# Kernel tuning notes

Hardware: AMD Instinct MI355X
Metric: run time of the kernel (lower is better)

Reference implementation:

```python
import jax, jax.numpy as jnp
import numpy as np

EPS_CLAMP = 1e-6
TAU2 = 1.0


def _l2norm_rows(x):
    # F.normalize(x, p=2, dim=1) with eps=1e-12
    n = jnp.sqrt(jnp.sum(x * x, axis=1, keepdims=True))
    return x / jnp.maximum(n, 1e-12)


def _ws_v22(x_mean, x_std):
    m = _l2norm_rows(x_mean)                      # [N, F]
    c = _l2norm_rows(jnp.exp(x_std))              # [N, F]
    sq = jnp.sum(m * m, axis=1)                   # [N]
    # squared euclidean pairwise distance (cdist(...)**2)
    d2 = jnp.maximum(sq[:, None] + sq[None, :] - 2.0 * (m @ m.T), 0.0)
    csum = jnp.sum(c, axis=1)                     # [N]
    cs = jnp.sqrt(c)
    res = d2 + csum[:, None] + csum[None, :] - 2.0 * (cs @ cs.T)
    return jnp.exp(-res)                          # [N, N]


def _gcn_conv_dense(A, x, W, b):
    # PyG GCNConv with dense weighted adjacency A (A[i,j] = weight of edge i->j),
    # add_remaining_self_loops(fill=1), deg over target (column sums),
    # norm_ij = d_i^-1/2 * A_ij * d_j^-1/2, aggregate at target: out = A_norm^T @ (xW) + b
    diag = jnp.diagonal(A)
    A = A + jnp.diag(jnp.where(diag > 0, 0.0, 1.0))  # add self-loop weight 1 only where missing
    deg = jnp.sum(A, axis=0)                         # column sums (target degree)
    dis = jnp.where(deg > 0, deg ** -0.5, 0.0)
    An = dis[:, None] * A * dis[None, :]
    return An.T @ (x @ W) + b


def _encoder(A, x, W0, b0, W1, b1):
    h = jax.nn.relu(_gcn_conv_dense(A, x, W0, b0))
    return jax.nn.relu(_gcn_conv_dense(A, h, W1, b1))


def setup_inputs() -> dict:
    key = jax.random.key(0)
    ks = jax.random.split(key, 16)
    N, F, H = 4096, 512, 256
    s_in = 1.0 / np.sqrt(F)
    s_h = 1.0 / np.sqrt(2 * H)
    inp = {
        "x": jax.random.normal(ks[0], (N, F), dtype=jnp.float32),
        "new_edge": jax.random.uniform(ks[1], (N, N), dtype=jnp.float32),
        "beta": jax.random.uniform(ks[2], (1,), dtype=jnp.float32),
        "delta": jax.random.uniform(ks[3], (1,), dtype=jnp.float32),
        "eps": jax.random.uniform(ks[4], (N, N), dtype=jnp.float32),
        "Wm": jax.random.uniform(ks[5], (F, F), jnp.float32, -s_in, s_in),
        "bm": jax.random.uniform(ks[6], (F,), jnp.float32, -s_in, s_in),
        "Ws": jax.random.uniform(ks[7], (F, F), jnp.float32, -s_in, s_in),
        "bs": jax.random.uniform(ks[8], (F,), jnp.float32, -s_in, s_in),
        "mW0": jax.random.uniform(ks[9], (F, 2 * H), jnp.float32, -s_in, s_in) ,
        "mb0": jnp.zeros((2 * H,), jnp.float32),
        "mW1": jax.random.uniform(ks[10], (2 * H, H), jnp.float32, -s_h, s_h),
        "mb1": jnp.zeros((H,), jnp.float32),
        "sW0": jax.random.uniform(ks[11], (F, 2 * H), jnp.float32, -s_in, s_in),
        "sb0": jnp.zeros((2 * H,), jnp.float32),
        "sW1": jax.random.uniform(ks[12], (2 * H, H), jnp.float32, -s_h, s_h),
        "sb1": jnp.zeros((H,), jnp.float32),
    }
    return inp


def reference(x, new_edge, beta, delta, eps, Wm, bm, Ws, bs,
              mW0, mb0, mW1, mb1, sW0, sb0, sW1, sb1):
    b = beta[0]
    d = delta[0]
    x_mean = x @ Wm + bm
    x_std = x @ Ws + bs
    ws = _l2norm_rows(_ws_v22(x_mean, x_std))       # F.normalize(WS_v22(...)) row-wise
    term = (1.0 - b) * ws + b * new_edge
    term = jnp.clip(term, EPS_CLAMP, 1.0 - EPS_CLAMP)
    term = jnp.log(term / (1.0 - term))
    e = jnp.clip(eps, EPS_CLAMP, 1.0 - EPS_CLAMP)
    term = term + jnp.log(e / (1.0 - e))
    term = jax.nn.sigmoid(term / TAU2)
    term = jnp.where(term > d, term, 0.0)           # dense sparsified adjacency
    z_mean = _encoder(term, x_mean, mW0, mb0, mW1, mb1)
    z_std = _encoder(term, x_std, sW0, sb0, sW1, sb1)
    return z_mean, z_std
```

## Files before the change

### kernel.cpp

```cpp
#include <hip/hip_runtime.h>
#include <cstddef>

static constexpr int kN = 4096;
static constexpr int kF = 512;
static constexpr int kH = 256;
static constexpr float kClamp = 1e-6f;

using bf16x8 = __attribute__((ext_vector_type(8))) __bf16;
using f32x4 = __attribute__((ext_vector_type(4))) float;
using ushort8 = __attribute__((ext_vector_type(8))) unsigned short;
using ushort4v = __attribute__((ext_vector_type(4))) unsigned short;

static constexpr size_t PLANE_XF = (size_t)kN * kF;
static constexpr size_t PLANE_NN = (size_t)kN * kN;
static constexpr size_t PLANE_W = (size_t)512 * 512;
static constexpr size_t PLANE_W1 = (size_t)256 * 512;
static constexpr size_t PLANE_V0 = (size_t)1024 * kN;
static constexpr size_t PLANE_H = (size_t)kN * 1024;
static constexpr size_t PLANE_V1 = (size_t)512 * kN;

__device__ __forceinline__ unsigned short f2bf(float x) {
  unsigned int u = __float_as_uint(x);
  u += 0x7fffu + ((u >> 16) & 1u);
  return (unsigned short)(u >> 16);
}
__device__ __forceinline__ float bf2f(unsigned short h) {
  return __uint_as_float(((unsigned int)h) << 16);
}
__device__ __forceinline__ void split3(float x, unsigned short& h,
                                       unsigned short& m, unsigned short& l) {
  h = f2bf(x);
  const float r1 = x - bf2f(h);
  m = f2bf(r1);
  l = f2bf(r1 - bf2f(m));
}
__device__ __forceinline__ void split2(float x, unsigned short& h,
                                       unsigned short& m) {
  h = f2bf(x);
  m = f2bf(x - bf2f(h));
}
__device__ __forceinline__ void split2x4(const float4 v, ushort4v& h4,
                                         ushort4v& m4) {
  unsigned short h, m;
  split2(v.x, h, m); h4.x = h; m4.x = m;
  split2(v.y, h, m); h4.y = h; m4.y = m;
  split2(v.z, h, m); h4.z = h; m4.z = m;
  split2(v.w, h, m); h4.w = h; m4.w = m;
}

__device__ __forceinline__ bf16x8 ldfrag(const unsigned short* p) {
  ushort8 r = *(const ushort8*)p;
  return __builtin_bit_cast(bf16x8, r);
}
__device__ __forceinline__ f32x4 mfma16(bf16x8 a, bf16x8 b, f32x4 c) {
  return __builtin_amdgcn_mfma_f32_16x16x32_bf16(a, b, c, 0, 0, 0);
}
__device__ __forceinline__ f32x4 mfma_split6(const bf16x8* a3, const bf16x8* b3,
                                             f32x4 acc) {
  acc = mfma16(a3[2], b3[0], acc);
  acc = mfma16(a3[0], b3[2], acc);
  acc = mfma16(a3[1], b3[1], acc);
  acc = mfma16(a3[1], b3[0], acc);
  acc = mfma16(a3[0], b3[1], acc);
  acc = mfma16(a3[0], b3[0], acc);
  return acc;
}

__device__ __forceinline__ void tri_map(int b, int& bi, int& bj) {
  int x = (int)((sqrtf(8.0f * (float)b + 1.0f) - 1.0f) * 0.5f);
  while ((x + 1) * (x + 2) / 2 <= b) ++x;
  while (x * (x + 1) / 2 > b) --x;
  bi = x;
  bj = b - x * (x + 1) / 2;
}

__device__ __forceinline__ float block_reduce_sum(float v, float* sbuf) {
  const int tid = threadIdx.x;
  sbuf[tid] = v;
  __syncthreads();
#pragma unroll
  for (int s = 128; s > 0; s >>= 1) {
    if (tid < s) sbuf[tid] += sbuf[tid + s];
    __syncthreads();
  }
  const float r = sbuf[0];
  __syncthreads();
  return r;
}

__global__ __launch_bounds__(256) void prep_w(
    const float* s0, const float* s1, const float* s2, const float* s3,
    const float* s4, const float* s5, unsigned short* d0, unsigned short* d1,
    unsigned short* d2, unsigned short* d3, unsigned short* d4,
    unsigned short* d5) {
  const int seg = blockIdx.y;
  const float* src;
  unsigned short* dst;
  int N;
  bool tri;
  switch (seg) {
    case 0: src = s0; dst = d0; N = 512; tri = true; break;
    case 1: src = s1; dst = d1; N = 512; tri = true; break;
    case 2: src = s2; dst = d2; N = 512; tri = false; break;
    case 3: src = s3; dst = d3; N = 512; tri = false; break;
    case 4: src = s4; dst = d4; N = 256; tri = false; break;
    default: src = s5; dst = d5; N = 256; tri = false; break;
  }
  const int id = blockIdx.x * 256 + threadIdx.x;
  if (id >= 512 * N) return;
  const int k = id & 511;
  const int n = id >> 9;
  const float v = src[(size_t)k * N + n];
  const size_t base = (size_t)n * 512 + k;
  const size_t plane = (size_t)512 * N;
  if (tri) {
    unsigned short h, m, l;
    split3(v, h, m, l);
    dst[base] = h;
    dst[plane + base] = m;
    dst[2 * plane + base] = l;
  } else {
    unsigned short h, m;
    split2(v, h, m);
    dst[base] = h;
    dst[plane + base] = m;
  }
}

__global__ __launch_bounds__(256) void split_x(const float* __restrict__ x,
                                               unsigned short* __restrict__ x3) {
  const size_t id = (size_t)blockIdx.x * 256 + threadIdx.x;
  unsigned short h, m, l;
  split3(x[id], h, m, l);
  x3[id] = h;
  x3[PLANE_XF + id] = m;
  x3[2 * PLANE_XF + id] = l;
}

__global__ __launch_bounds__(256) void gemm_x(
    const unsigned short* __restrict__ A3, const unsigned short* __restrict__ B30,
    const unsigned short* __restrict__ B31, float* __restrict__ C0,
    float* __restrict__ C1, const float* __restrict__ bias0,
    const float* __restrict__ bias1) {
  constexpr int BM = 128, BN = 64, K = 512;
  __shared__ __align__(16) unsigned short Asl[3][BM][40];
  __shared__ __align__(16) unsigned short Bsl[3][BN][40];
  const int tid = threadIdx.x;
  const int lane = tid & 63;
  const int wave = tid >> 6;
  const int wm = wave >> 1, wn = wave & 1;
  const int m0 = blockIdx.y * BM;
  const int n0 = blockIdx.x * BN;
  const bool str1 = (n0 >= 512);
  const int nloc = str1 ? (n0 - 512) : n0;
  const unsigned short* Bb = str1 ? B31 : B30;
  const float* bias = str1 ? bias1 : bias0;
  float* C = str1 ? C1 : C0;
  const int rl = lane & 15;
  const int kq = (lane >> 4) * 8;
  const int q = lane >> 4;

  f32x4 acc[4][2];
#pragma unroll
  for (int i = 0; i < 4; ++i)
#pragma unroll
    for (int j = 0; j < 2; ++j) acc[i][j] = (f32x4){0.f, 0.f, 0.f, 0.f};

  for (int k0 = 0; k0 < K; k0 += 32) {
#pragma unroll
    for (int it = 0; it < 6; ++it) {
      const int c = tid + it * 256;
      const int plane = c / (BM * 4);
      const int rem = c % (BM * 4);
      const int row = rem >> 2;
      const int kc = (rem & 3) * 8;
      const ushort8 v = *(const ushort8*)(&A3[(size_t)plane * PLANE_XF +
                                              (size_t)(m0 + row) * K + k0 + kc]);
      *(ushort8*)(&Asl[plane][row][kc]) = v;
    }
#pragma unroll
    for (int it = 0; it < 3; ++it) {
      const int c = tid + it * 256;
      const int plane = c / (BN * 4);
      const int rem = c % (BN * 4);
      const int row = rem >> 2;
      const int kc = (rem & 3) * 8;
      const ushort8 v = *(const ushort8*)(&Bb[(size_t)plane * PLANE_W +
                                              (size_t)(nloc + row) * K + k0 + kc]);
      *(ushort8*)(&Bsl[plane][row][kc]) = v;
    }
    __syncthreads();
    bf16x8 af[4][3], bfr[2][3];
#pragma unroll
    for (int mt = 0; mt < 4; ++mt)
#pragma unroll
      for (int t = 0; t < 3; ++t)
        af[mt][t] = ldfrag(&Asl[t][wm * 64 + mt * 16 + rl][kq]);
#pragma unroll
    for (int nt = 0; nt < 2; ++nt)
#pragma unroll
      for (int t = 0; t < 3; ++t)
        bfr[nt][t] = ldfrag(&Bsl[t][wn * 32 + nt * 16 + rl][kq]);
#pragma unroll
    for (int mt = 0; mt < 4; ++mt)
#pragma unroll
      for (int nt = 0; nt < 2; ++nt)
        acc[mt][nt] = mfma_split6(af[mt], bfr[nt], acc[mt][nt]);
    __syncthreads();
  }
#pragma unroll
  for (int mt = 0; mt < 4; ++mt)
#pragma unroll
    for (int nt = 0; nt < 2; ++nt) {
      const int col = nloc + wn * 32 + nt * 16 + rl;
      const int row0 = m0 + wm * 64 + mt * 16 + q * 4;
      const float bv = bias[col];
#pragma unroll
      for (int r = 0; r < 4; ++r)
        C[(size_t)(row0 + r) * 512 + col] = acc[mt][nt][r] + bv;
    }
}

template <int BM, int BN>
__global__ __launch_bounds__(256) void gemm2ct(
    const unsigned short* __restrict__ A0, const unsigned short* __restrict__ A1,
    int lda, size_t planeA, const unsigned short* __restrict__ B0,
    const unsigned short* __restrict__ B1, int ldb, size_t planeB,
    unsigned short* __restrict__ Cs0, unsigned short* __restrict__ Cs1, int ldc,
    size_t planeC, int N1, int K, const float* __restrict__ rowScale) {
  __shared__ __align__(16) unsigned short Asl[2][BM][40];
  __shared__ __align__(16) unsigned short Bsl[2][BN][40];
  const int tid = threadIdx.x;
  const int lane = tid & 63;
  const int wave = tid >> 6;
  const int wm = wave >> 1, wn = wave & 1;
  const int m0 = blockIdx.y * BM;
  const int n0 = blockIdx.x * BN;
  const bool str1 = (n0 >= N1);
  const int nloc = str1 ? (n0 - N1) : n0;
  const unsigned short* Ab = str1 ? A1 : A0;
  const unsigned short* Bb = str1 ? B1 : B0;
  const int rl = lane & 15;
  const int kq = (lane >> 4) * 8;
  const int q = lane >> 4;
  constexpr int MT = BM / 32;
  constexpr int NT = BN / 32;

  f32x4 acc[MT][NT];
#pragma unroll
  for (int i = 0; i < MT; ++i)
#pragma unroll
    for (int j = 0; j < NT; ++j) acc[i][j] = (f32x4){0.f, 0.f, 0.f, 0.f};

  for (int k0 = 0; k0 < K; k0 += 32) {
    constexpr int AIT = (2 * BM * 4) / 256;
#pragma unroll
    for (int it = 0; it < AIT; ++it) {
      const int c = tid + it * 256;
      const int plane = c / (BM * 4);
      const int rem = c % (BM * 4);
      const int row = rem >> 2;
      const int kc = (rem & 3) * 8;
      const ushort8 v = *(const ushort8*)(&Ab[(size_t)plane * planeA +
                                              (size_t)(m0 + row) * lda + k0 + kc]);
      *(ushort8*)(&Asl[plane][row][kc]) = v;
    }
    constexpr int BIT = (2 * BN * 4) / 256;
#pragma unroll
    for (int it = 0; it < BIT; ++it) {
      const int c = tid + it * 256;
      const int plane = c / (BN * 4);
      const int rem = c % (BN * 4);
      const int row = rem >> 2;
      const int kc = (rem & 3) * 8;
      const ushort8 v = *(const ushort8*)(&Bb[(size_t)plane * planeB +
                                              (size_t)(nloc + row) * ldb + k0 + kc]);
      *(ushort8*)(&Bsl[plane][row][kc]) = v;
    }
    __syncthreads();
    bf16x8 af[MT][2];
#pragma unroll
    for (int mt = 0; mt < MT; ++mt)
#pragma unroll
      for (int t = 0; t < 2; ++t)
        af[mt][t] = ldfrag(&Asl[t][wm * (BM / 2) + mt * 16 + rl][kq]);
#pragma unroll
    for (int nt = 0; nt < NT; ++nt) {
      const bf16x8 b0 = ldfrag(&Bsl[0][wn * (BN / 2) + nt * 16 + rl][kq]);
      const bf16x8 b1 = ldfrag(&Bsl[1][wn * (BN / 2) + nt * 16 + rl][kq]);
#pragma unroll
      for (int mt = 0; mt < MT; ++mt) {
        acc[mt][nt] = mfma16(af[mt][1], b0, acc[mt][nt]);
        acc[mt][nt] = mfma16(af[mt][0], b1, acc[mt][nt]);
        acc[mt][nt] = mfma16(af[mt][0], b0, acc[mt][nt]);
      }
    }
    __syncthreads();
  }

#pragma unroll
  for (int mt = 0; mt < MT; ++mt) {
#pragma unroll
    for (int nt = 0; nt < NT; ++nt) {
      const int colL = nloc + wn * (BN / 2) + nt * 16 + rl;
      const int row0 = m0 + wm * (BM / 2) + mt * 16 + q * 4;
      float4 v4;
      float* vp = &v4.x;
#pragma unroll
      for (int r = 0; r < 4; ++r) {
        float v = acc[mt][nt][r];
        if (rowScale) v *= rowScale[row0 + r];
        vp[r] = v;
      }
      unsigned short* C = str1 ? Cs1 : Cs0;
      ushort4v h4, m4;
      split2x4(v4, h4, m4);
      const size_t base = (size_t)colL * ldc + row0;
      *(ushort4v*)(&C[base]) = h4;
      *(ushort4v*)(&C[planeC + base]) = m4;
    }
  }
}

template <int BM, int BN, int GX, int GYP, int GZ>
__global__ __launch_bounds__(256) void gemm2k(
    const unsigned short* __restrict__ A, int lda, size_t planeA,
    const unsigned short* __restrict__ B, int ldb, size_t planeB,
    float* __restrict__ Cp, int ldc, int Mtot, int Ksl) {
  __shared__ __align__(16) unsigned short Asl[2][BM][40];
  __shared__ __align__(16) unsigned short Bsl[2][BN][40];
  const int lin = blockIdx.x;
  const int xcd = lin & 7;
  const int s = lin >> 3;
  constexpr int per = GX * GYP;
  const int z = s / per;
  const int r = s - z * per;
  const int bx = r % GX;
  const int by = xcd * GYP + r / GX;
  const int m0 = by * BM;
  const int n0 = bx * BN;
  const int kOff = z * Ksl;

  const int tid = threadIdx.x;
  const int lane = tid & 63;
  const int wave = tid >> 6;
  const int wm = wave >> 1, wn = wave & 1;
  const int rl = lane & 15;
  const int kq = (lane >> 4) * 8;
  const int q = lane >> 4;
  constexpr int MT = BM / 32;
  constexpr int NT = BN / 32;

  f32x4 acc[MT][NT];
#pragma unroll
  for (int i = 0; i < MT; ++i)
#pragma unroll
    for (int j = 0; j < NT; ++j) acc[i][j] = (f32x4){0.f, 0.f, 0.f, 0.f};

  for (int k0 = 0; k0 < Ksl; k0 += 32) {
    constexpr int AIT = (2 * BM * 4) / 256;
#pragma unroll
    for (int it = 0; it < AIT; ++it) {
      const int c = tid + it * 256;
      const int plane = c / (BM * 4);
      const int rem = c % (BM * 4);
      const int row = rem >> 2;
      const int kc = (rem & 3) * 8;
      const ushort8 v = *(const ushort8*)(&A[(size_t)plane * planeA +
                                             (size_t)(m0 + row) * lda + kOff +
                                             k0 + kc]);
      *(ushort8*)(&Asl[plane][row][kc]) = v;
    }
    constexpr int BIT = (2 * BN * 4) / 256;
#pragma unroll
    for (int it = 0; it < BIT; ++it) {
      const int c = tid + it * 256;
      const int plane = c / (BN * 4);
      const int rem = c % (BN * 4);
      const int row = rem >> 2;
      const int kc = (rem & 3) * 8;
      const ushort8 v = *(const ushort8*)(&B[(size_t)plane * planeB +
                                             (size_t)(n0 + row) * ldb + kOff +
                                             k0 + kc]);
      *(ushort8*)(&Bsl[plane][row][kc]) = v;
    }
    __syncthreads();
    bf16x8 af[MT][2];
#pragma unroll
    for (int mt = 0; mt < MT; ++mt)
#pragma unroll
      for (int t = 0; t < 2; ++t)
        af[mt][t] = ldfrag(&Asl[t][wm * (BM / 2) + mt * 16 + rl][kq]);
#pragma unroll
    for (int nt = 0; nt < NT; ++nt) {
      const bf16x8 b0 = ldfrag(&Bsl[0][wn * (BN / 2) + nt * 16 + rl][kq]);
      const bf16x8 b1 = ldfrag(&Bsl[1][wn * (BN / 2) + nt * 16 + rl][kq]);
#pragma unroll
      for (int mt = 0; mt < MT; ++mt) {
        acc[mt][nt] = mfma16(af[mt][1], b0, acc[mt][nt]);
        acc[mt][nt] = mfma16(af[mt][0], b1, acc[mt][nt]);
        acc[mt][nt] = mfma16(af[mt][0], b0, acc[mt][nt]);
      }
    }
    __syncthreads();
  }

  const size_t zoff = (size_t)z * (size_t)Mtot * (size_t)ldc;
#pragma unroll
  for (int mt = 0; mt < MT; ++mt) {
#pragma unroll
    for (int nt = 0; nt < NT; ++nt) {
      const int colL = n0 + wn * (BN / 2) + nt * 16 + rl;
      const int row0 = m0 + wm * (BM / 2) + mt * 16 + q * 4;
#pragma unroll
      for (int r = 0; r < 4; ++r)
        Cp[zoff + (size_t)(row0 + r) * ldc + colL] = acc[mt][nt][r];
    }
  }
}

__global__ __launch_bounds__(256) void row_stats(
    const float* __restrict__ XMf, const float* __restrict__ XSf,
    unsigned short* __restrict__ M2, unsigned short* __restrict__ CS2,
    unsigned short* __restrict__ XM2, unsigned short* __restrict__ XS2,
    float* __restrict__ sq, float* __restrict__ csum) {
  __shared__ float sbuf[256];
  const int i = blockIdx.x;
  const int tid = threadIdx.x;
  const size_t base = (size_t)i * kF;
  const size_t i0 = base + tid, i1 = base + tid + 256;
  const float x0 = XMf[i0], x1 = XMf[i1];
  {
    unsigned short h, m;
    split2(x0, h, m);
    XM2[i0] = h; XM2[PLANE_XF + i0] = m;
    split2(x1, h, m);
    XM2[i1] = h; XM2[PLANE_XF + i1] = m;
  }
  const float nrm = block_reduce_sum(x0 * x0 + x1 * x1, sbuf);
  const float inv = 1.0f / fmaxf(sqrtf(nrm), 1e-12f);
  const float m0 = x0 * inv, m1 = x1 * inv;
  {
    unsigned short h, m;
    split2(m0, h, m);
    M2[i0] = h; M2[PLANE_XF + i0] = m;
    split2(m1, h, m);
    M2[i1] = h; M2[PLANE_XF + i1] = m;
  }
  const float s2 = block_reduce_sum(m0 * m0 + m1 * m1, sbuf);
  if (tid == 0) sq[i] = s2;

  const float y0 = XSf[i0], y1 = XSf[i1];
  {
    unsigned short h, m;
    split2(y0, h, m);
    XS2[i0] = h; XS2[PLANE_XF + i0] = m;
    split2(y1, h, m);
    XS2[i1] = h; XS2[PLANE_XF + i1] = m;
  }
  const float e0 = expf(y0), e1 = expf(y1);
  const float nrm2 = block_reduce_sum(e0 * e0 + e1 * e1, sbuf);
  const float inv2 = 1.0f / fmaxf(sqrtf(nrm2), 1e-12f);
  const float c0 = e0 * inv2, c1 = e1 * inv2;
  const float sc = block_reduce_sum(c0 + c1, sbuf);
  if (tid == 0) csum[i] = sc;
  {
    unsigned short h, m;
    split2(sqrtf(c0), h, m);
    CS2[i0] = h; CS2[PLANE_XF + i0] = m;
    split2(sqrtf(c1), h, m);
    CS2[i1] = h; CS2[PLANE_XF + i1] = m;
  }
}

__global__ __launch_bounds__(256) void ws_mfma2(
    const unsigned short* __restrict__ M2, const unsigned short* __restrict__ CS2,
    const float* __restrict__ sq, const float* __restrict__ csum,
    float* __restrict__ WSR) {
  __shared__ __align__(16) unsigned short S[4][2][64][40];
  int bi, bj;
  tri_map(blockIdx.x, bi, bj);
  const int i0 = bi * 64, j0 = bj * 64;
  const int tid = threadIdx.x;
  const int lane = tid & 63;
  const int wave = tid >> 6;
  const int wm = wave >> 1, wn = wave & 1;
  const int rl = lane & 15;
  const int kq = (lane >> 4) * 8;
  const int q = lane >> 4;

  f32x4 aM[2][2], aC[2][2];
#pragma unroll
  for (int i = 0; i < 2; ++i)
#pragma unroll
    for (int j = 0; j < 2; ++j) {
      aM[i][j] = (f32x4){0.f, 0.f, 0.f, 0.f};
      aC[i][j] = (f32x4){0.f, 0.f, 0.f, 0.f};
    }

  for (int k0 = 0; k0 < kF; k0 += 32) {
#pragma unroll
    for (int it = 0; it < 8; ++it) {
      const int c = tid + it * 256;
      const int op = c >> 9;
      const int rem = c & 511;
      const int plane = rem >> 8;
      const int r2 = rem & 255;
      const int row = r2 >> 2;
      const int kc = (r2 & 3) * 8;
      const unsigned short* mat = (op & 1) ? CS2 : M2;
      const int rowoff = (op < 2) ? i0 : j0;
      const ushort8 v = *(const ushort8*)(&mat[(size_t)plane * PLANE_XF +
                                               (size_t)(rowoff + row) * kF + k0 +
                                               kc]);
      *(ushort8*)(&S[op][plane][row][kc]) = v;
    }
    __syncthreads();
    bf16x8 am[2][2], ac[2][2], bm[2][2], bc[2][2];
#pragma unroll
    for (int mt = 0; mt < 2; ++mt)
#pragma unroll
      for (int t = 0; t < 2; ++t) {
        am[mt][t] = ldfrag(&S[0][t][wm * 32 + mt * 16 + rl][kq]);
        ac[mt][t] = ldfrag(&S[1][t][wm * 32 + mt * 16 + rl][kq]);
      }
#pragma unroll
    for (int nt = 0; nt < 2; ++nt)
#pragma unroll
      for (int t = 0; t < 2; ++t) {
        bm[nt][t] = ldfrag(&S[2][t][wn * 32 + nt * 16 + rl][kq]);
        bc[nt][t] = ldfrag(&S[3][t][wn * 32 + nt * 16 + rl][kq]);
      }
#pragma unroll
    for (int mt = 0; mt < 2; ++mt)
#pragma unroll
      for (int nt = 0; nt < 2; ++nt) {
        aM[mt][nt] = mfma16(am[mt][1], bm[nt][0], aM[mt][nt]);
        aM[mt][nt] = mfma16(am[mt][0], bm[nt][1], aM[mt][nt]);
        aM[mt][nt] = mfma16(am[mt][0], bm[nt][0], aM[mt][nt]);
        aC[mt][nt] = mfma16(ac[mt][1], bc[nt][0], aC[mt][nt]);
        aC[mt][nt] = mfma16(ac[mt][0], bc[nt][1], aC[mt][nt]);
        aC[mt][nt] = mfma16(ac[mt][0], bc[nt][0], aC[mt][nt]);
      }
    __syncthreads();
  }

#pragma unroll
  for (int mt = 0; mt < 2; ++mt) {
#pragma unroll
    for (int nt = 0; nt < 2; ++nt) {
      const int j = j0 + wn * 32 + nt * 16 + rl;
      const int ib = i0 + wm * 32 + mt * 16 + q * 4;
      const float sqj = sq[j], csj = csum[j];
      float4 vv;
      float* vp = &vv.x;
#pragma unroll
      for (int r = 0; r < 4; ++r) {
        const int i = ib + r;
        const float d2 = fmaxf(sq[i] + sqj - 2.0f * aM[mt][nt][r], 0.0f);
        const float res = d2 + csum[i] + csj - 2.0f * aC[mt][nt][r];
        const float v = expf(-res);
        vp[r] = v;
        WSR[(size_t)i * kN + j] = v;
      }
      if (bi != bj) *(float4*)(&WSR[(size_t)j * kN + ib]) = vv;
    }
  }
}

__global__ __launch_bounds__(256) void row_invnorm_kernel(
    const float* __restrict__ WSR, float* __restrict__ invn) {
  __shared__ float sbuf[256];
  const int i = blockIdx.x;
  const int tid = threadIdx.x;
  const float4* rp = (const float4*)(WSR + (size_t)i * kN);
  float s = 0.0f;
#pragma unroll
  for (int q = 0; q < (kN / 4) / 256; ++q) {
    const float4 v = rp[tid + q * 256];
    s += v.x * v.x + v.y * v.y + v.z * v.z + v.w * v.w;
  }
  s = block_reduce_sum(s, sbuf);
  if (tid == 0) invn[i] = 1.0f / fmaxf(sqrtf(s), 1e-12f);
}

__device__ __forceinline__ float adj_val(float w, float inv, float nev, float ev,
                                         float b, float d, bool diag) {
  float t = (1.0f - b) * (w * inv) + b * nev;
  t = fminf(fmaxf(t, kClamp), 1.0f - kClamp);
  float L = logf(t / (1.0f - t));
  const float e = fminf(fmaxf(ev, kClamp), 1.0f - kClamp);
  L += logf(e / (1.0f - e));
  const float s = 1.0f / (1.0f + expf(-L));
  float v = (s > d) ? s : 0.0f;
  if (diag) v = (v > 0.0f) ? v : 1.0f;
  return v;
}

__global__ __launch_bounds__(256) void adj_transpose(
    const float* __restrict__ WSR, const float* __restrict__ invn,
    const float* __restrict__ ne, const float* __restrict__ epsm,
    const float* __restrict__ beta_p, const float* __restrict__ delta_p,
    unsigned short* __restrict__ Adj2, float* __restrict__ degp) {
  __shared__ float T0[64][65];
  __shared__ float T1[64][65];
  const float b = beta_p[0];
  const float d = delta_p[0];
  int bi, bj;
  tri_map(blockIdx.x, bi, bj);
  const int i0 = bi * 64, j0 = bj * 64;
  const int tid = threadIdx.x;
  const int rlq = tid >> 4;
  const int cq = (tid & 15) * 4;
#pragma unroll
  for (int p = 0; p < 4; ++p) {
    const int ii = p * 16 + rlq;
    {
      const size_t off = (size_t)(i0 + ii) * kN + j0 + cq;
      const float4 w4 = *(const float4*)(&WSR[off]);
      const float4 n4 = *(const float4*)(&ne[off]);
      const float4 e4 = *(const float4*)(&epsm[off]);
      const float inv = invn[i0 + ii];
      const float wv[4] = {w4.x, w4.y, w4.z, w4.w};
      const float nv[4] = {n4.x, n4.y, n4.z, n4.w};
      const float ev[4] = {e4.x, e4.y, e4.z, e4.w};
#pragma unroll
      for (int u = 0; u < 4; ++u)
        T0[ii][cq + u] =
            adj_val(wv[u], inv, nv[u], ev[u], b, d, (i0 + ii) == (j0 + cq + u));
    }
    if (bi != bj) {
      const size_t off = (size_t)(j0 + ii) * kN + i0 + cq;
      const float4 w4 = *(const float4*)(&WSR[off]);
      const float4 n4 = *(const float4*)(&ne[off]);
      const float4 e4 = *(const float4*)(&epsm[off]);
      const float inv = invn[j0 + ii];
      const float wv[4] = {w4.x, w4.y, w4.z, w4.w};
      const float nv[4] = {n4.x, n4.y, n4.z, n4.w};
      const float ev[4] = {e4.x, e4.y, e4.z, e4.w};
#pragma unroll
      for (int u = 0; u < 4; ++u)
        T1[ii][cq + u] = adj_val(wv[u], inv, nv[u], ev[u], b, d, false);
    }
  }
  __syncthreads();
#pragma unroll
  for (int p = 0; p < 4; ++p) {
    const int jj = p * 16 + rlq;
    {
      const float4 v4 = make_float4(T0[cq + 0][jj], T0[cq + 1][jj],
                                    T0[cq + 2][jj], T0[cq + 3][jj]);
      ushort4v h4, m4;
      split2x4(v4, h4, m4);
      const size_t base = (size_t)(j0 + jj) * kN + i0 + cq;
      *(ushort4v*)(&Adj2[base]) = h4;
      *(ushort4v*)(&Adj2[PLANE_NN + base]) = m4;
    }
    if (bi != bj) {
      const float4 v4 = make_float4(T1[cq + 0][jj], T1[cq + 1][jj],
                                    T1[cq + 2][jj], T1[cq + 3][jj]);
      ushort4v h4, m4;
      split2x4(v4, h4, m4);
      const size_t base = (size_t)(i0 + jj) * kN + j0 + cq;
      *(ushort4v*)(&Adj2[base]) = h4;
      *(ushort4v*)(&Adj2[PLANE_NN + base]) = m4;
    }
  }
  if (tid < 64) {
    float s = 0.0f;
#pragma unroll 8
    for (int ii = 0; ii < 64; ++ii) s += T0[ii][tid];
    degp[(size_t)bi * kN + j0 + tid] = s;
    if (bi != bj) {
      float s1 = 0.0f;
#pragma unroll 8
      for (int ii = 0; ii < 64; ++ii) s1 += T1[ii][tid];
      degp[(size_t)bj * kN + i0 + tid] = s1;
    }
  }
}

__global__ __launch_bounds__(256) void deg_dis_kernel(
    const float* __restrict__ degp, float* __restrict__ dis) {
  const int j = blockIdx.x * 256 + threadIdx.x;
  float s = 0.0f;
#pragma unroll
  for (int c = 0; c < 64; ++c) s += degp[(size_t)c * kN + j];
  dis[j] = (s > 0.0f) ? (1.0f / sqrtf(s)) : 0.0f;
}

__global__ __launch_bounds__(256) void combine_h(
    const float* __restrict__ hp, const float* __restrict__ dis,
    const float* __restrict__ b0, const float* __restrict__ b1,
    unsigned short* __restrict__ h2) {
  const size_t qd = (size_t)blockIdx.x * 256 + threadIdx.x;
  const int m = (int)(qd >> 8);
  const int c0 = (int)(qd & 255) * 4;
  const size_t off = (size_t)m * 1024 + c0;
  const float4 s0 = *(const float4*)(&hp[off]);
  const float4 s1 = *(const float4*)(&hp[PLANE_H + off]);
  const float4 s2 = *(const float4*)(&hp[2 * PLANE_H + off]);
  const float4 s3 = *(const float4*)(&hp[3 * PLANE_H + off]);
  const float4 bv = (c0 < 512) ? *(const float4*)(&b0[c0])
                               : *(const float4*)(&b1[c0 - 512]);
  const float ds = dis[m];
  float4 v4;
  v4.x = fmaxf(ds * (s0.x + s1.x + s2.x + s3.x) + bv.x, 0.f);
  v4.y = fmaxf(ds * (s0.y + s1.y + s2.y + s3.y) + bv.y, 0.f);
  v4.z = fmaxf(ds * (s0.z + s1.z + s2.z + s3.z) + bv.z, 0.f);
  v4.w = fmaxf(ds * (s0.w + s1.w + s2.w + s3.w) + bv.w, 0.f);
  ushort4v h4, m4;
  split2x4(v4, h4, m4);
  *(ushort4v*)(&h2[off]) = h4;
  *(ushort4v*)(&h2[PLANE_H + off]) = m4;
}

__global__ __launch_bounds__(256) void combine_z(
    const float* __restrict__ zp, const float* __restrict__ dis,
    const float* __restrict__ b0, const float* __restrict__ b1,
    float* __restrict__ out) {
  const size_t qd = (size_t)blockIdx.x * 256 + threadIdx.x;
  const int m = (int)(qd >> 7);
  const int c0 = (int)(qd & 127) * 4;
  const size_t off = (size_t)m * 512 + c0;
  constexpr size_t PZ = (size_t)kN * 512;
  const float4 s0 = *(const float4*)(&zp[off]);
  const float4 s1 = *(const float4*)(&zp[PZ + off]);
  const float4 s2 = *(const float4*)(&zp[2 * PZ + off]);
  const float4 s3 = *(const float4*)(&zp[3 * PZ + off]);
  const float4 bv = (c0 < 256) ? *(const float4*)(&b0[c0])
                               : *(const float4*)(&b1[c0 - 256]);
  const float ds = dis[m];
  float4 v4;
  v4.x = fmaxf(ds * (s0.x + s1.x + s2.x + s3.x) + bv.x, 0.f);
  v4.y = fmaxf(ds * (s0.y + s1.y + s2.y + s3.y) + bv.y, 0.f);
  v4.z = fmaxf(ds * (s0.z + s1.z + s2.z + s3.z) + bv.z, 0.f);
  v4.w = fmaxf(ds * (s0.w + s1.w + s2.w + s3.w) + bv.w, 0.f);
  float* dst = (c0 < 256) ? &out[(size_t)m * 256 + c0]
                          : &out[(size_t)kN * 256 + (size_t)m * 256 + (c0 - 256)];
  *(float4*)dst = v4;
}

extern "C" void kernel_launch(void* const* d_in, const int* in_sizes, int n_in,
                              void* d_out, int out_size, void* d_ws,
                              size_t ws_size, hipStream_t stream) {
  const float* x = (const float*)d_in[0];
  const float* ne = (const float*)d_in[1];
  const float* beta = (const float*)d_in[2];
  const float* delta = (const float*)d_in[3];
  const float* epsm = (const float*)d_in[4];
  const float* Wm = (const float*)d_in[5];
  const float* bm = (const float*)d_in[6];
  const float* Ws = (const float*)d_in[7];
  const float* bs = (const float*)d_in[8];
  const float* mW0 = (const float*)d_in[9];
  const float* mb0 = (const float*)d_in[10];
  const float* mW1 = (const float*)d_in[11];
  const float* mb1 = (const float*)d_in[12];
  const float* sW0 = (const float*)d_in[13];
  const float* sb0 = (const float*)d_in[14];
  const float* sW1 = (const float*)d_in[15];
  const float* sb1 = (const float*)d_in[16];
  float* out = (float*)d_out;

  char* p = (char*)d_ws;
  float* WSR = (float*)p;                     p += PLANE_NN * 4;
  unsigned short* Adj2 = (unsigned short*)p;  p += 2 * PLANE_NN * 2;
  unsigned short* x3 = (unsigned short*)p;    p += 3 * PLANE_XF * 2;
  float* XMf = (float*)p;                     p += PLANE_XF * 4;
  float* XSf = (float*)p;                     p += PLANE_XF * 4;
  unsigned short* XM2 = (unsigned short*)p;   p += 2 * PLANE_XF * 2;
  unsigned short* XS2 = (unsigned short*)p;   p += 2 * PLANE_XF * 2;
  unsigned short* M2 = (unsigned short*)p;    p += 2 * PLANE_XF * 2;
  unsigned short* CS2 = (unsigned short*)p;   p += 2 * PLANE_XF * 2;
  unsigned short* Wm3 = (unsigned short*)p;   p += 3 * PLANE_W * 2;
  unsigned short* Ws3 = (unsigned short*)p;   p += 3 * PLANE_W * 2;
  unsigned short* mW0t2 = (unsigned short*)p; p += 2 * PLANE_W * 2;
  unsigned short* sW0t2 = (unsigned short*)p; p += 2 * PLANE_W * 2;
  unsigned short* mW1t2 = (unsigned short*)p; p += 2 * PLANE_W1 * 2;
  unsigned short* sW1t2 = (unsigned short*)p; p += 2 * PLANE_W1 * 2;
  float* degp = (float*)p;                    p += (size_t)64 * kN * 4;
  float* sq = (float*)p;                      p += kN * 4;
  float* csum = (float*)p;                    p += kN * 4;
  float* invn = (float*)p;                    p += kN * 4;
  float* dis = (float*)p;                     p += kN * 4;

  float* hp = WSR;
  float* zp = WSR;
  unsigned short* V1t2 = x3;
  unsigned short* h2 = XM2;
  unsigned short* V0t2 = M2;

  const dim3 blk(256);
  const int nTri = (kN / 64) * (kN / 64 + 1) / 2;

  prep_w<<<dim3(1024, 6), blk, 0, stream>>>(Wm, Ws, mW0, sW0, mW1, sW1, Wm3,
                                            Ws3, mW0t2, sW0t2, mW1t2, sW1t2);
  split_x<<<(kN * kF) / 256, blk, 0, stream>>>(x, x3);

  gemm_x<<<dim3(16, 32), blk, 0, stream>>>(x3, Wm3, Ws3, XMf, XSf, bm, bs);

  row_stats<<<kN, blk, 0, stream>>>(XMf, XSf, M2, CS2, XM2, XS2, sq, csum);

  ws_mfma2<<<nTri, blk, 0, stream>>>(M2, CS2, sq, csum, WSR);

  row_invnorm_kernel<<<kN, blk, 0, stream>>>(WSR, invn);

  adj_transpose<<<nTri, blk, 0, stream>>>(WSR, invn, ne, epsm, beta, delta,
                                          Adj2, degp);
  deg_dis_kernel<<<kN / 256, blk, 0, stream>>>(degp, dis);

  gemm2ct<128, 64><<<dim3(16, 32), blk, 0, stream>>>(
      XM2, XS2, kF, PLANE_XF, mW0t2, sW0t2, kF, PLANE_W, V0t2,
      V0t2 + (size_t)512 * kN, kN, PLANE_V0, 512, kF, dis);

  gemm2k<128, 128, 8, 4, 4><<<1024, blk, 0, stream>>>(
      Adj2, kN, PLANE_NN, V0t2, kN, PLANE_V0, hp, 1024, kN, kN / 4);
  combine_h<<<(int)(PLANE_H / 4 / 256), blk, 0, stream>>>(hp, dis, mb0, sb0, h2);

  gemm2ct<64, 64><<<dim3(8, 64), blk, 0, stream>>>(
      h2, h2 + 512, 1024, PLANE_H, mW1t2, sW1t2, kF, PLANE_W1, V1t2,
      V1t2 + (size_t)256 * kN, kN, PLANE_V1, 256, kF, dis);

  gemm2k<128, 128, 4, 4, 4><<<512, blk, 0, stream>>>(
      Adj2, kN, PLANE_NN, V1t2, kN, PLANE_V1, zp, 512, kN, kN / 4);
  combine_z<<<(int)((size_t)kN * 512 / 4 / 256), blk, 0, stream>>>(zp, dis, mb1,
                                                                   sb1, out);
}
```

Measured before the change: 636.2 us.

## Enlarge WS tile to 128, fuse row-norm partials, raise split-K for second aggregation

The similarity kernel now computes 128x128 triangular tiles and accumulates squared row and column sums into shared memory. It writes per-tile partial sums so a tiny kernel can produce the row inverse norms without rereading the full NxN matrix. The second adjacency GEMM doubles its split-K factor to 8 for more blocks, and combine_z sums eight partial planes. This trades extra registers, shared-memory atomics and more partial-output traffic for a removed full-matrix read pass and better occupancy.

```diff
diff --git a/kernel.cpp b/kernel.cpp
--- a/kernel.cpp
+++ b/kernel.cpp
@@ -473,14 +473,14 @@
   }
 }
 
-__global__ __launch_bounds__(256) void ws_mfma2(
+__global__ __launch_bounds__(256, 2) void ws_mfma2(
     const unsigned short* __restrict__ M2, const unsigned short* __restrict__ CS2,
     const float* __restrict__ sq, const float* __restrict__ csum,
-    float* __restrict__ WSR) {
-  __shared__ __align__(16) unsigned short S[4][2][64][40];
+    float* __restrict__ WSR, float* __restrict__ rsqp) {
+  __shared__ __align__(16) unsigned short S[4][2][128][40];
   int bi, bj;
   tri_map(blockIdx.x, bi, bj);
-  const int i0 = bi * 64, j0 = bj * 64;
+  const int i0 = bi * 128, j0 = bj * 128;
   const int tid = threadIdx.x;
   const int lane = tid & 63;
   const int wave = tid >> 6;
@@ -489,23 +489,23 @@
   const int kq = (lane >> 4) * 8;
   const int q = lane >> 4;
 
-  f32x4 aM[2][2], aC[2][2];
-#pragma unroll
-  for (int i = 0; i < 2; ++i)
-#pragma unroll
-    for (int j = 0; j < 2; ++j) {
+  f32x4 aM[4][4], aC[4][4];
+#pragma unroll
+  for (int i = 0; i < 4; ++i)
+#pragma unroll
+    for (int j = 0; j < 4; ++j) {
       aM[i][j] = (f32x4){0.f, 0.f, 0.f, 0.f};
       aC[i][j] = (f32x4){0.f, 0.f, 0.f, 0.f};
     }
 
   for (int k0 = 0; k0 < kF; k0 += 32) {
 #pragma unroll
-    for (int it = 0; it < 8; ++it) {
+    for (int it = 0; it < 16; ++it) {
       const int c = tid + it * 256;
-      const int op = c >> 9;
-      const int rem = c & 511;
-      const int plane = rem >> 8;
-      const int r2 = rem & 255;
+      const int op = c >> 10;
+      const int rem = c & 1023;
+      const int plane = rem >> 9;
+      const int r2 = rem & 511;
       const int row = r2 >> 2;
       const int kc = (r2 & 3) * 8;
       const unsigned short* mat = (op & 1) ? CS2 : M2;
@@ -516,41 +516,71 @@
       *(ushort8*)(&S[op][plane][row][kc]) = v;
     }
     __syncthreads();
-    bf16x8 am[2][2], ac[2][2], bm[2][2], bc[2][2];
-#pragma unroll
-    for (int mt = 0; mt < 2; ++mt)
-#pragma unroll
-      for (int t = 0; t < 2; ++t) {
-        am[mt][t] = ldfrag(&S[0][t][wm * 32 + mt * 16 + rl][kq]);
-        ac[mt][t] = ldfrag(&S[1][t][wm * 32 + mt * 16 + rl][kq]);
-      }
-#pragma unroll
-    for (int nt = 0; nt < 2; ++nt)
-#pragma unroll
-      for (int t = 0; t < 2; ++t) {
-        bm[nt][t] = ldfrag(&S[2][t][wn * 32 + nt * 16 + rl][kq]);
-        bc[nt][t] = ldfrag(&S[3][t][wn * 32 + nt * 16 + rl][kq]);
-      }
-#pragma unroll
-    for (int mt = 0; mt < 2; ++mt)
-#pragma unroll
-      for (int nt = 0; nt < 2; ++nt) {
-        aM[mt][nt] = mfma16(am[mt][1], bm[nt][0], aM[mt][nt]);
-        aM[mt][nt] = mfma16(am[mt][0], bm[nt][1], aM[mt][nt]);
-        aM[mt][nt] = mfma16(am[mt][0], bm[nt][0], aM[mt][nt]);
-        aC[mt][nt] = mfma16(ac[mt][1], bc[nt][0], aC[mt][nt]);
-        aC[mt][nt] = mfma16(ac[mt][0], bc[nt][1], aC[mt][nt]);
-        aC[mt][nt] = mfma16(ac[mt][0], bc[nt][0], aC[mt][nt]);
-      }
+    {
+      bf16x8 a_[4][2], b_[4][2];
+#pragma unroll
+      for (int mt = 0; mt < 4; ++mt)
+#pragma unroll
+        for (int t = 0; t < 2; ++t)
+          a_[mt][t] = ldfrag(&S[0][t][wm * 64 + mt * 16 + rl][kq]);
+#pragma unroll
+      for (int nt = 0; nt < 4; ++nt)
+#pragma unroll
+        for (int t = 0; t < 2; ++t)
+          b_[nt][t] = ldfrag(&S[2][t][wn * 64 + nt * 16 + rl][kq]);
+#pragma unroll
+      for (int mt = 0; mt < 4; ++mt)
+#pragma unroll
+        for (int nt = 0; nt < 4; ++nt) {
+          aM[mt][nt] = mfma16(a_[mt][1], b_[nt][0], aM[mt][nt]);
+          aM[mt][nt] = mfma16(a_[mt][0], b_[nt][1], aM[mt][nt]);
+          aM[mt][nt] = mfma16(a_[mt][0], b_[nt][0], aM[mt][nt]);
+        }
+    }
+    {
+      bf16x8 a_[4][2], b_[4][2];
+#pragma unroll
+      for (int mt = 0; mt < 4; ++mt)
+#pragma unroll
+        for (int t = 0; t < 2; ++t)
+          a_[mt][t] = ldfrag(&S[1][t][wm * 64 + mt * 16 + rl][kq]);
+#pragma unroll
+      for (int nt = 0; nt < 4; ++nt)
+#pragma unroll
+        for (int t = 0; t < 2; ++t)
+          b_[nt][t] = ldfrag(&S[3][t][wn * 64 + nt * 16 + rl][kq]);
+#pragma unroll
+      for (int mt = 0; mt < 4; ++mt)
+#pragma unroll
+        for (int nt = 0; nt < 4; ++nt) {
+          aC[mt][nt] = mfma16(a_[mt][1], b_[nt][0], aC[mt][nt]);
+          aC[mt][nt] = mfma16(a_[mt][0], b_[nt][1], aC[mt][nt]);
+          aC[mt][nt] = mfma16(a_[mt][0], b_[nt][0], aC[mt][nt]);
+        }
+    }
     __syncthreads();
   }
 
-#pragma unroll
-  for (int mt = 0; mt < 2; ++mt) {
-#pragma unroll
-    for (int nt = 0; nt < 2; ++nt) {
-      const int j = j0 + wn * 32 + nt * 16 + rl;
-      const int ib = i0 + wm * 32 + mt * 16 + q * 4;
+  float* rs_ = (float*)&S[0][0][0][0];
+  float* cs_ = rs_ + 128;
+  if (tid < 256) rs_[tid] = 0.f;
+  __syncthreads();
+
+  float rowacc[4][4];
+  float colacc[4];
+#pragma unroll
+  for (int i = 0; i < 4; ++i) {
+    colacc[i] = 0.f;
+#pragma unroll
+    for (int j = 0; j < 4; ++j) rowacc[i][j] = 0.f;
+  }
+
+#pragma unroll
+  for (int mt = 0; mt < 4; ++mt) {
+#pragma unroll
+    for (int nt = 0; nt < 4; ++nt) {
+      const int j = j0 + wn * 64 + nt * 16 + rl;
+      const int ib = i0 + wm * 64 + mt * 16 + q * 4;
       const float sqj = sq[j], csj = csum[j];
       float4 vv;
       float* vp = &vv.x;
@@ -562,26 +592,34 @@
         const float v = expf(-res);
         vp[r] = v;
         WSR[(size_t)i * kN + j] = v;
+        rowacc[mt][r] += v * v;
+        colacc[nt] += v * v;
       }
       if (bi != bj) *(float4*)(&WSR[(size_t)j * kN + ib]) = vv;
     }
   }
-}
-
-__global__ __launch_bounds__(256) void row_invnorm_kernel(
-    const float* __restrict__ WSR, float* __restrict__ invn) {
-  __shared__ float sbuf[256];
-  const int i = blockIdx.x;
-  const int tid = threadIdx.x;
-  const float4* rp = (const float4*)(WSR + (size_t)i * kN);
+#pragma unroll
+  for (int mt = 0; mt < 4; ++mt)
+#pragma unroll
+    for (int r = 0; r < 4; ++r)
+      atomicAdd(&rs_[wm * 64 + mt * 16 + q * 4 + r], rowacc[mt][r]);
+#pragma unroll
+  for (int nt = 0; nt < 4; ++nt)
+    atomicAdd(&cs_[wn * 64 + nt * 16 + rl], colacc[nt]);
+  __syncthreads();
+  if (tid < 128) {
+    rsqp[(size_t)bj * kN + i0 + tid] = rs_[tid];
+    if (bi != bj) rsqp[(size_t)bi * kN + j0 + tid] = cs_[tid];
+  }
+}
+
+__global__ __launch_bounds__(256) void invn_from_rsqp(
+    const float* __restrict__ rsqp, float* __restrict__ invn) {
+  const int i = blockIdx.x * 256 + threadIdx.x;
   float s = 0.0f;
 #pragma unroll
-  for (int q = 0; q < (kN / 4) / 256; ++q) {
-    const float4 v = rp[tid + q * 256];
-    s += v.x * v.x + v.y * v.y + v.z * v.z + v.w * v.w;
-  }
-  s = block_reduce_sum(s, sbuf);
-  if (tid == 0) invn[i] = 1.0f / fmaxf(sqrtf(s), 1e-12f);
+  for (int c = 0; c < 32; ++c) s += rsqp[(size_t)c * kN + i];
+  invn[i] = 1.0f / fmaxf(sqrtf(s), 1e-12f);
 }
 
 __device__ __forceinline__ float adj_val(float w, float inv, float nev, float ev,
@@ -724,18 +762,20 @@
   const int c0 = (int)(qd & 127) * 4;
   const size_t off = (size_t)m * 512 + c0;
   constexpr size_t PZ = (size_t)kN * 512;
-  const float4 s0 = *(const float4*)(&zp[off]);
-  const float4 s1 = *(const float4*)(&zp[PZ + off]);
-  const float4 s2 = *(const float4*)(&zp[2 * PZ + off]);
-  const float4 s3 = *(const float4*)(&zp[3 * PZ + off]);
+  float4 acc = make_float4(0.f, 0.f, 0.f, 0.f);
+#pragma unroll
+  for (int s = 0; s < 8; ++s) {
+    const float4 v = *(const float4*)(&zp[(size_t)s * PZ + off]);
+    acc.x += v.x; acc.y += v.y; acc.z += v.z; acc.w += v.w;
+  }
   const float4 bv = (c0 < 256) ? *(const float4*)(&b0[c0])
                                : *(const float4*)(&b1[c0 - 256]);
   const float ds = dis[m];
   float4 v4;
-  v4.x = fmaxf(ds * (s0.x + s1.x + s2.x + s3.x) + bv.x, 0.f);
-  v4.y = fmaxf(ds * (s0.y + s1.y + s2.y + s3.y) + bv.y, 0.f);
-  v4.z = fmaxf(ds * (s0.z + s1.z + s2.z + s3.z) + bv.z, 0.f);
-  v4.w = fmaxf(ds * (s0.w + s1.w + s2.w + s3.w) + bv.w, 0.f);
+  v4.x = fmaxf(ds * acc.x + bv.x, 0.f);
+  v4.y = fmaxf(ds * acc.y + bv.y, 0.f);
+  v4.z = fmaxf(ds * acc.z + bv.z, 0.f);
+  v4.w = fmaxf(ds * acc.w + bv.w, 0.f);
   float* dst = (c0 < 256) ? &out[(size_t)m * 256 + c0]
                           : &out[(size_t)kN * 256 + (size_t)m * 256 + (c0 - 256)];
   *(float4*)dst = v4;
@@ -780,6 +820,7 @@
   unsigned short* mW1t2 = (unsigned short*)p; p += 2 * PLANE_W1 * 2;
   unsigned short* sW1t2 = (unsigned short*)p; p += 2 * PLANE_W1 * 2;
   float* degp = (float*)p;                    p += (size_t)64 * kN * 4;
+  float* rsqp = (float*)p;                    p += (size_t)32 * kN * 4;
   float* sq = (float*)p;                      p += kN * 4;
   float* csum = (float*)p;                    p += kN * 4;
   float* invn = (float*)p;                    p += kN * 4;
@@ -792,7 +833,8 @@
   unsigned short* V0t2 = M2;
 
   const dim3 blk(256);
-  const int nTri = (kN / 64) * (kN / 64 + 1) / 2;
+  const int nTri64 = (kN / 64) * (kN / 64 + 1) / 2;
+  const int nTri128 = (kN / 128) * (kN / 128 + 1) / 2;
 
   prep_w<<<dim3(1024, 6), blk, 0, stream>>>(Wm, Ws, mW0, sW0, mW1, sW1, Wm3,
                                             Ws3, mW0t2, sW0t2, mW1t2, sW1t2);
@@ -802,12 +844,12 @@
 
   row_stats<<<kN, blk, 0, stream>>>(XMf, XSf, M2, CS2, XM2, XS2, sq, csum);
 
-  ws_mfma2<<<nTri, blk, 0, stream>>>(M2, CS2, sq, csum, WSR);
-
-  row_invnorm_kernel<<<kN, blk, 0, stream>>>(WSR, invn);
-
-  adj_transpose<<<nTri, blk, 0, stream>>>(WSR, invn, ne, epsm, beta, delta,
-                                          Adj2, degp);
+  ws_mfma2<<<nTri128, blk, 0, stream>>>(M2, CS2, sq, csum, WSR, rsqp);
+
+  invn_from_rsqp<<<kN / 256, blk, 0, stream>>>(rsqp, invn);
+
+  adj_transpose<<<nTri64, blk, 0, stream>>>(WSR, invn, ne, epsm, beta, delta,
+                                            Adj2, degp);
   deg_dis_kernel<<<kN / 256, blk, 0, stream>>>(degp, dis);
 
   gemm2ct<128, 64><<<dim3(16, 32), blk, 0, stream>>>(
@@ -822,8 +864,8 @@
       h2, h2 + 512, 1024, PLANE_H, mW1t2, sW1t2, kF, PLANE_W1, V1t2,
       V1t2 + (size_t)256 * kN, kN, PLANE_V1, 256, kF, dis);
 
-  gemm2k<128, 128, 4, 4, 4><<<512, blk, 0, stream>>>(
-      Adj2, kN, PLANE_NN, V1t2, kN, PLANE_V1, zp, 512, kN, kN / 4);
+  gemm2k<128, 128, 4, 4, 8><<<1024, blk, 0, stream>>>(
+      Adj2, kN, PLANE_NN, V1t2, kN, PLANE_V1, zp, 512, kN, kN / 8);
   combine_z<<<(int)((size_t)kN * 512 / 4 / 256), blk, 0, stream>>>(zp, dis, mb1,
                                                                    sb1, out);
 }
```

Result: slower. 712.2 us (+11.9%).
